# Kernel optimization log

Hardware: AMD Instinct MI355X
Metric: run time of the kernel (lower is better)

The kernel has to match this reference:

```python
import jax, jax.numpy as jnp
import numpy as np

DIM = 2          # num_input_channels
NB = 8           # num_bins (normflows default)
TB = 3.0         # tail_bound
MINW = 1e-3; MINH = 1e-3; MIND = 1e-3
H = 128          # hidden_units
NL = 16          # flow_length
NBLK = 2         # hidden_layers (MADE residual blocks)
PM = 3 * NB - 1  # spline params per dim
DCONST = float(np.log(np.expm1(1.0 - MIND)))  # tail pad constant for derivatives
SQH = float(np.sqrt(H))
LU_EPS = 1e-3

# MADE masks for features=2: input degrees [1,2], all hidden degrees = 1
_M0 = np.zeros((H, DIM), np.float32); _M0[:, 0] = 1.0
_MF = np.zeros((DIM * PM, H), np.float32); _MF[PM:, :] = 1.0
M0 = jnp.asarray(_M0); MF = jnp.asarray(_MF)


def _mlp(x, w1, b1, w2, b2):
    return jax.nn.silu(x @ w1.T + b1) @ w2.T + b2


def _made(zin, W0, b0, Wres, bres, Wf, bf):
    h = zin @ (W0 * M0).T + b0
    for blk in range(NBLK):  # residual blocks (hidden masks all-ones for dim=2)
        t = jax.nn.relu(h)
        t = t @ Wres[blk, 0].T + bres[blk, 0]
        t = jax.nn.relu(t)
        t = t @ Wres[blk, 1].T + bres[blk, 1]
        h = h + t
    return (h @ (Wf * MF).T + bf).reshape(zin.shape[0], DIM, PM)


def _rqs_inverse(y, uw, uh, ud):
    # unconstrained rational-quadratic spline with linear tails, inverse direction
    widths = MINW + (1 - MINW * NB) * jax.nn.softmax(uw, -1)
    cw = jnp.concatenate([jnp.zeros_like(widths[..., :1]), jnp.cumsum(widths, -1)], -1)
    cw = (2 * TB * cw - TB).at[..., 0].set(-TB).at[..., -1].set(TB)
    widths = cw[..., 1:] - cw[..., :-1]
    heights = MINH + (1 - MINH * NB) * jax.nn.softmax(uh, -1)
    ch = jnp.concatenate([jnp.zeros_like(heights[..., :1]), jnp.cumsum(heights, -1)], -1)
    ch = (2 * TB * ch - TB).at[..., 0].set(-TB).at[..., -1].set(TB)
    heights = ch[..., 1:] - ch[..., :-1]
    pad = jnp.full(ud.shape[:-1] + (1,), DCONST, ud.dtype)
    d = MIND + jax.nn.softplus(jnp.concatenate([pad, ud, pad], -1))
    inside = (y >= -TB) & (y <= TB)
    yc = jnp.clip(y, -TB, TB)
    idx = jnp.clip(jnp.sum(yc[..., None] >= ch, -1) - 1, 0, NB - 1)[..., None]
    take = lambda a, i: jnp.take_along_axis(a, i, -1)[..., 0]
    yk = take(ch, idx); hk = take(heights, idx)
    xk = take(cw, idx); wk = take(widths, idx)
    dk = take(d, idx); dk1 = take(d, idx + 1)
    sk = hk / wk; dy = yc - yk; t2 = dk + dk1 - 2 * sk
    a = dy * t2 + hk * (sk - dk)
    b = hk * dk - dy * t2
    c = -sk * dy
    disc = jnp.maximum(b * b - 4 * a * c, 0.0)
    theta = 2 * c / (-b - jnp.sqrt(disc))
    xo = theta * wk + xk
    om = 1 - theta
    denom = sk + t2 * theta * om
    dnum = (sk * sk) * (dk1 * theta * theta + 2 * sk * theta * om + dk * om * om)
    ld_fwd = jnp.log(dnum) - 2 * jnp.log(denom)
    return jnp.where(inside, xo, y), jnp.where(inside, -ld_fwd, 0.0)


def _flow_forward(z_0, x, sigma, n1_w1, n1_b1, n1_w2, n1_b2, n2_w1, n2_b1, n2_w2, n2_b2,
                  made_W0, made_b0, made_Wres, made_bres, made_Wf, made_bf,
                  lu_lower, lu_upper, lu_diag, lu_bias, perms):
    tcond = _mlp(sigma, n1_w1, n1_b1, n1_w2, n1_b2)
    z = _mlp(jnp.concatenate([z_0, x], -1), n2_w1, n2_b1, n2_w2, n2_b2) + tcond
    ld_tot = jnp.zeros(z.shape[0], z.dtype)
    for i in range(NL):
        # AR RQ-spline flow: flow.forward() == sequential inverse of MADE spline
        y = z
        out = jnp.zeros_like(y)
        ldp = jnp.zeros_like(y)
        for _ in range(DIM):
            p = _made(out, made_W0[i], made_b0[i], made_Wres[i], made_bres[i], made_Wf[i], made_bf[i])
            out, ldp = _rqs_inverse(y, p[..., :NB] / SQH, p[..., NB:2 * NB] / SQH, p[..., 2 * NB:])
        ld_tot = ld_tot + ldp.sum(-1)
        # LULinearPermute.forward == LU-linear inverse then permutation inverse
        diag = jax.nn.softplus(lu_diag[i]) + LU_EPS
        Lm = jnp.eye(DIM, dtype=z.dtype).at[1, 0].set(lu_lower[i])
        Um = jnp.diag(diag).at[0, 1].set(lu_upper[i])
        Wm = Lm @ Um
        z = (out - lu_bias[i]) @ jnp.linalg.inv(Wm).T
        ld_tot = ld_tot - jnp.sum(jnp.log(diag))
        z = z[:, perms[i]]
    return z, ld_tot


def setup_inputs() -> dict:
    key = jax.random.key(0)
    ks = jax.random.split(key, 20)
    B = 262144
    f = jnp.float32
    rn = lambda k, s, sc=1.0: jax.random.normal(k, s, dtype=f) * sc
    inp = {}
    inp["z_0"] = rn(ks[0], (B, DIM))
    inp["x"] = rn(ks[1], (B, DIM))
    inp["sigma"] = jax.random.uniform(ks[2], (B, 1), dtype=f)
    inp["n1_w1"] = rn(ks[3], (32, 1), 0.5); inp["n1_b1"] = jnp.zeros((32,), f)
    inp["n1_w2"] = rn(ks[4], (DIM, 32), 0.2); inp["n1_b2"] = jnp.zeros((DIM,), f)
    inp["n2_w1"] = rn(ks[5], (32, 2 * DIM), 0.5); inp["n2_b1"] = jnp.zeros((32,), f)
    inp["n2_w2"] = rn(ks[6], (DIM, 32), 0.2); inp["n2_b2"] = jnp.zeros((DIM,), f)
    inp["made_W0"] = rn(ks[7], (NL, H, DIM), 0.3)
    inp["made_b0"] = rn(ks[8], (NL, H), 0.1)
    inp["made_Wres"] = rn(ks[9], (NL, NBLK, 2, H, H), 0.05)
    inp["made_bres"] = rn(ks[10], (NL, NBLK, 2, H), 0.05)
    inp["made_Wf"] = rn(ks[11], (NL, DIM * PM, H), 0.05)
    inp["made_bf"] = rn(ks[12], (NL, DIM * PM), 0.05)
    inp["lu_lower"] = rn(ks[13], (NL,), 0.3)
    inp["lu_upper"] = rn(ks[14], (NL,), 0.3)
    inp["lu_diag"] = rn(ks[15], (NL, DIM), 0.3) + 0.5413  # softplus^-1(1)
    inp["lu_bias"] = rn(ks[16], (NL, DIM), 0.1)
    inp["perms"] = jnp.asarray(np.stack([[1, 0] if i % 2 else [0, 1] for i in range(NL)]).astype(np.int32))
    return inp


def reference(z_0, x, sigma, n1_w1, n1_b1, n1_w2, n1_b2, n2_w1, n2_b1, n2_w2, n2_b2,
              made_W0, made_b0, made_Wres, made_bres, made_Wf, made_bf,
              lu_lower, lu_upper, lu_diag, lu_bias, perms):
    return _flow_forward(z_0, x, sigma, n1_w1, n1_b1, n1_w2, n1_b2, n2_w1, n2_b1, n2_w2, n2_b2,
                         made_W0, made_b0, made_Wres, made_bres, made_Wf, made_bf,
                         lu_lower, lu_upper, lu_diag, lu_bias, perms)
```

## Files before the change

### kernel.cpp

```cpp
#include <hip/hip_runtime.h>
#include <math.h>

#define NBATCH 262144
#define INVSQH 0.08838834764831845f

#define NPT   2048
#define NGRID 1920
#define TROW  24

#define WT_OFF   0
#define WFT_OFF  4194304
#define WS0_OFF  4456448
#define XS_OFF   4464640
#define BP_OFF   4472832
#define TAB_OFF  4603904
#define REC_OFF  7749632
#define LDC_OFF  7752192

__device__ __forceinline__ float fastrcp(float x) {
#if __has_builtin(__builtin_amdgcn_rcpf)
    return __builtin_amdgcn_rcpf(x);
#else
    return 1.f / x;
#endif
}
__device__ __forceinline__ float fastdiv(float a, float b) { return a * fastrcp(b); }
__device__ __forceinline__ float fastsqrt(float x) {
#if __has_builtin(__builtin_amdgcn_sqrtf)
    return __builtin_amdgcn_sqrtf(x);
#else
    return sqrtf(x);
#endif
}

__device__ __forceinline__ float softplusf(float x) {
    return (x > 15.f) ? x : __logf(1.f + __expf(x));
}

__device__ __forceinline__ float gridval(int i) {
    float v = -56.8f + i * 0.25f;
    if (i >= 192)  v = -8.8f + (i - 192) * 0.0125f;
    if (i >= 1600) v = 9.05f + (i - 1600) * 0.25f;
    if (i >= 1792) v = 58.5f + (i - 1792) * 0.01f;
    return v;
}
__device__ __forceinline__ int cnt_grid_le_exact(float x) {
    int c = 0;
#pragma unroll
    for (int stp = 1024; stp; stp >>= 1) {
        int n = c + stp;
        if (n <= NGRID && gridval(n - 1) <= x) c = n;
    }
    return c;
}
__device__ __forceinline__ int cnt_grid_le_fast(float x) {
    if (x < -56.8f) return 0;
    if (x < -8.8f)  return min((int)floorf((x + 56.8f) * 4.0f) + 1, 192);
    if (x < 9.05f)  return 192 + min((int)floorf((x + 8.8f) * 80.0f) + 1, 1408);
    if (x < 58.5f)  return 1600 + min((int)floorf((x - 9.05f) * 4.0f) + 1, 192);
    return 1792 + min((int)floorf((x - 58.5f) * 100.0f) + 1, 128);
}

__device__ __forceinline__ void rqs_solve(float y, float yc, float yk, float hk, float xk,
                                          float wk, float dk, float dk1,
                                          float& xout, float& ldout)
{
    float sk = fastdiv(hk, wk);
    float dy = yc - yk;
    float t2 = dk + dk1 - 2.f * sk;
    float av = dy * t2 + hk * (sk - dk);
    float bv = hk * dk - dy * t2;
    float cv = -sk * dy;
    float disc = fmaxf(bv * bv - 4.f * av * cv, 0.f);
    float theta = 2.f * cv * fastrcp(-bv - fastsqrt(disc));
    float xo = fmaf(theta, wk, xk);
    float om = 1.f - theta;
    float denom = fmaf(t2, theta * om, sk);
    float dnum = sk * sk * (dk1 * theta * theta + 2.f * sk * theta * om + dk * om * om);
    float rden = fastrcp(denom);
    float ldf = __logf(dnum * rden * rden);
    bool inside = (y >= -3.f) && (y <= 3.f);
    xout  = inside ? xo : y;
    ldout = inside ? -ldf : 0.f;
}

__device__ __forceinline__ void knots_from_p(const float* __restrict__ p,
                                             float* __restrict__ cw,
                                             float* __restrict__ ch,
                                             float* __restrict__ d)
{
    float uw[8], uh[8];
#pragma unroll
    for (int j = 0; j < 8; ++j) uw[j] = p[j] * INVSQH;
#pragma unroll
    for (int j = 0; j < 8; ++j) uh[j] = p[8 + j] * INVSQH;
    float mw = uw[0], mh = uh[0];
#pragma unroll
    for (int j = 1; j < 8; ++j) { mw = fmaxf(mw, uw[j]); mh = fmaxf(mh, uh[j]); }
    float ew[8], eh[8], sw = 0.f, sh = 0.f;
#pragma unroll
    for (int j = 0; j < 8; ++j) {
        ew[j] = __expf(uw[j] - mw); sw += ew[j];
        eh[j] = __expf(uh[j] - mh); sh += eh[j];
    }
    float isw = 0.992f * fastrcp(sw), ish = 0.992f * fastrcp(sh);
    cw[0] = -3.f; ch[0] = -3.f;
    float aw = 0.f, ah = 0.f;
#pragma unroll
    for (int j = 0; j < 8; ++j) {
        aw += 0.001f + ew[j] * isw;
        ah += 0.001f + eh[j] * ish;
        cw[j + 1] = 6.f * aw - 3.f;
        ch[j + 1] = 6.f * ah - 3.f;
    }
    cw[8] = 3.f; ch[8] = 3.f;
    d[0] = 1.f; d[8] = 1.f;
#pragma unroll
    for (int j = 0; j < 7; ++j) d[j + 1] = 0.001f + softplusf(p[16 + j]);
}

__device__ __forceinline__ void rqs_from_knots(float y, const float* __restrict__ cw,
                                               const float* __restrict__ ch,
                                               const float* __restrict__ d,
                                               float& xout, float& ldout)
{
    float yc = fminf(fmaxf(y, -3.f), 3.f);
    float yk = ch[0], hk = ch[1] - ch[0], xk = cw[0], wk = cw[1] - cw[0];
    float dk = d[0], dk1 = d[1];
#pragma unroll
    for (int j = 1; j < 8; ++j) {
        bool cge = (yc >= ch[j]);
        yk  = cge ? ch[j] : yk;
        hk  = cge ? (ch[j + 1] - ch[j]) : hk;
        xk  = cge ? cw[j] : xk;
        wk  = cge ? (cw[j + 1] - cw[j]) : wk;
        dk  = cge ? d[j] : dk;
        dk1 = cge ? d[j + 1] : dk1;
    }
    rqs_solve(y, yc, yk, hk, xk, wk, dk, dk1, xout, ldout);
}

__device__ __forceinline__ void rqs_knots(float y, const float* __restrict__ rec,
                                          float& xout, float& ldout)
{
    rqs_from_knots(y, rec, rec + 9, rec + 18, xout, ldout);
}

extern "C" __global__ __launch_bounds__(256)
void nsf_prep(const float* __restrict__ Wresg, const float* __restrict__ Wfg,
              const float* __restrict__ W0g,  const float* __restrict__ b0g,
              const float* __restrict__ bfg,
              const float* __restrict__ lulg, const float* __restrict__ luug,
              const float* __restrict__ ludg, const float* __restrict__ lubg,
              const int* __restrict__ permsg, char* __restrict__ ws)
{
    const int t = blockIdx.x * 256 + threadIdx.x;
    const int stride = gridDim.x * 256;
    float* WT  = (float*)(ws + WT_OFF);
    float* WFT = (float*)(ws + WFT_OFF);
    float* ws0 = (float*)(ws + WS0_OFF);
    float* xsg = (float*)(ws + XS_OFF);
    float* bp  = (float*)(ws + BP_OFF);

    for (int e = t; e < 16 * 4 * 16384; e += stride) {
        int sidx = e >> 14, rem = e & 16383, k = rem >> 7, u = rem & 127;
        WT[e] = Wresg[sidx * 16384 + u * 128 + k];
    }
    for (int e = t; e < 16 * 128 * 32; e += stride) {
        int L = e >> 12, rem = e & 4095, k = rem >> 5, o = rem & 31;
        WFT[e] = (o < 23) ? Wfg[(L * 46 + 23 + o) * 128 + k] : 0.f;
    }
    for (int e = t; e < 2048; e += stride) ws0[e] = W0g[2 * e];

    if (blockIdx.x < 16) {
        __shared__ float xr[128], xsL[128];
        const int L = blockIdx.x, tid = threadIdx.x;
        if (tid < 128) {
            float aa = W0g[L * 256 + 2 * tid];
            float cc = b0g[L * 128 + tid];
            float xv = -cc / aa;
            xr[tid] = (fabsf(xv) < 56.0f) ? xv : (57.0f + tid * 0.01f);
        }
        __syncthreads();
        if (tid < 128) {
            float v = xr[tid];
            int rank = 0;
            for (int j = 0; j < 128; ++j) {
                float u = xr[j];
                rank += (u < v || (u == v && j < tid)) ? 1 : 0;
            }
            xsL[rank] = v;
        }
        __syncthreads();
        if (tid < 128) {
            float v = xsL[tid];
            xsg[L * 128 + tid] = v;
            bp[L * NPT + tid + cnt_grid_le_exact(v)] = v;
        }
        for (int i = tid; i < NGRID; i += 256) {
            float g = gridval(i);
            int cl = 0;
#pragma unroll
            for (int stp = 64; stp; stp >>= 1)
                if (xsL[cl + stp - 1] < g) cl += stp;
            bp[L * NPT + i + cl] = g;
        }
        if (tid == 0) {
            float* rec = (float*)(ws + REC_OFF) + L * 40;
            const float* p = bfg + L * 46;
            for (int half = 0; half < 2; ++half) {
                float u[8], m = -1e30f;
                for (int j = 0; j < 8; ++j) { u[j] = p[half * 8 + j] * INVSQH; m = fmaxf(m, u[j]); }
                float e[8], ssum = 0.f;
                for (int j = 0; j < 8; ++j) { e[j] = expf(u[j] - m); ssum += e[j]; }
                float cum = 0.f;
                rec[half * 9 + 0] = -3.f;
                for (int j = 0; j < 8; ++j) {
                    cum += 0.001f + 0.992f * e[j] / ssum;
                    rec[half * 9 + 1 + j] = 6.f * cum - 3.f;
                }
                rec[half * 9 + 8] = 3.f;
            }
            rec[18] = 1.f; rec[26] = 1.f;
            for (int j = 0; j < 7; ++j) {
                float x = p[16 + j];
                rec[19 + j] = 0.001f + ((x > 15.f) ? x : log1pf(expf(x)));
            }
            float x0 = ludg[2 * L], x1 = ludg[2 * L + 1];
            float dg0 = 0.001f + ((x0 > 15.f) ? x0 : log1pf(expf(x0)));
            float dg1 = 0.001f + ((x1 > 15.f) ? x1 : log1pf(expf(x1)));
            float ll = lulg[L], uu = luug[L];
            float det = dg0 * dg1;
            float c00 = (ll * uu + dg1) / det, c01 = -uu / det;
            float c10 = -ll / dg1, c11 = 1.f / dg1;
            int pa = permsg[2 * L], pb = permsg[2 * L + 1];
            rec[27] = pa ? c10 : c00; rec[28] = pa ? c11 : c01;
            rec[29] = pb ? c10 : c00; rec[30] = pb ? c11 : c01;
            rec[31] = lubg[2 * L];    rec[32] = lubg[2 * L + 1];
        }
        if (L == 0 && tid == 32) {
            float ssum = 0.f;
            for (int l2 = 0; l2 < 16; ++l2) {
                float x0 = ludg[2 * l2], x1 = ludg[2 * l2 + 1];
                float dg0 = 0.001f + ((x0 > 15.f) ? x0 : log1pf(expf(x0)));
                float dg1 = 0.001f + ((x1 > 15.f) ? x1 : log1pf(expf(x1)));
                ssum += logf(dg0) + logf(dg1);
            }
            *(float*)(ws + LDC_OFF) = ssum;
        }
    }
}

extern "C" __global__ __launch_bounds__(256, 2)
void nsf_eval(const float* __restrict__ bresg, const float* __restrict__ b0g,
              const float* __restrict__ bfg, char* __restrict__ ws)
{
    __shared__ float R[128 * 68];
    __shared__ float p1sh[64 * 24];
    const int tid = threadIdx.x;
    const int lane = tid & 63, w = tid >> 6;
    const int u0 = w * 32 + (lane & 3) * 8;
    const int p0 = (lane >> 2) * 4;
    const int L = blockIdx.x >> 5;
    const int pb = (blockIdx.x & 31) << 6;

    const float* WT  = (const float*)(ws + WT_OFF);
    const float* WFT = (const float*)(ws + WFT_OFF);
    const float* ws0 = (const float*)(ws + WS0_OFF);
    const float* bp  = (const float*)(ws + BP_OFF);
    float* tab = (float*)(ws + TAB_OFF);

    float H[8][4];
    {
        float4 s4 = *(const float4*)(bp + L * NPT + pb + p0);
        float sp[4] = {s4.x, s4.y, s4.z, s4.w};
        float4 a0 = *(const float4*)(ws0 + L * 128 + u0);
        float4 a1 = *(const float4*)(ws0 + L * 128 + u0 + 4);
        float4 c0 = *(const float4*)(b0g + L * 128 + u0);
        float4 c1 = *(const float4*)(b0g + L * 128 + u0 + 4);
        float aj[8] = {a0.x, a0.y, a0.z, a0.w, a1.x, a1.y, a1.z, a1.w};
        float cj[8] = {c0.x, c0.y, c0.z, c0.w, c1.x, c1.y, c1.z, c1.w};
#pragma unroll
        for (int j = 0; j < 8; ++j) {
#pragma unroll
            for (int p = 0; p < 4; ++p) H[j][p] = fmaf(aj[j], sp[p], cj[j]);
            float4 v = {fmaxf(H[j][0], 0.f), fmaxf(H[j][1], 0.f),
                        fmaxf(H[j][2], 0.f), fmaxf(H[j][3], 0.f)};
            *(float4*)(&R[(u0 + j) * 68 + p0]) = v;
        }
    }
    __syncthreads();

#pragma unroll 1
    for (int st = 0; st < 4; ++st) {
        const float* Wst = WT + (L * 4 + st) * 16384;
        const float* bb  = bresg + (L * 4 + st) * 128;
        float acc[8][4];
        {
            float4 b0v = *(const float4*)(bb + u0);
            float4 b1v = *(const float4*)(bb + u0 + 4);
            float bj[8] = {b0v.x, b0v.y, b0v.z, b0v.w, b1v.x, b1v.y, b1v.z, b1v.w};
#pragma unroll
            for (int j = 0; j < 8; ++j)
#pragma unroll
                for (int p = 0; p < 4; ++p) acc[j][p] = bj[j];
        }
#pragma unroll 4
        for (int k = 0; k < 128; ++k) {
            float4 w0 = *(const float4*)(Wst + k * 128 + u0);
            float4 w1 = *(const float4*)(Wst + k * 128 + u0 + 4);
            float4 r  = *(const float4*)(&R[k * 68 + p0]);
            float wj[8] = {w0.x, w0.y, w0.z, w0.w, w1.x, w1.y, w1.z, w1.w};
            float rp[4] = {r.x, r.y, r.z, r.w};
#pragma unroll
            for (int j = 0; j < 8; ++j)
#pragma unroll
                for (int p = 0; p < 4; ++p)
                    acc[j][p] = fmaf(wj[j], rp[p], acc[j][p]);
        }
        if (st == 1 || st == 3) {
#pragma unroll
            for (int j = 0; j < 8; ++j)
#pragma unroll
                for (int p = 0; p < 4; ++p) H[j][p] += acc[j][p];
        }
        __syncthreads();
#pragma unroll
        for (int j = 0; j < 8; ++j) {
            float4 v;
            if (st == 0 || st == 2) {
                v = (float4){fmaxf(acc[j][0], 0.f), fmaxf(acc[j][1], 0.f),
                             fmaxf(acc[j][2], 0.f), fmaxf(acc[j][3], 0.f)};
            } else if (st == 1) {
                v = (float4){fmaxf(H[j][0], 0.f), fmaxf(H[j][1], 0.f),
                             fmaxf(H[j][2], 0.f), fmaxf(H[j][3], 0.f)};
            } else {
                v = (float4){H[j][0], H[j][1], H[j][2], H[j][3]};
            }
            *(float4*)(&R[(u0 + j) * 68 + p0]) = v;
        }
        __syncthreads();
    }

    {
        const int o = tid & 31, pg8 = tid >> 5;
        float pacc[8];
#pragma unroll
        for (int p = 0; p < 8; ++p) pacc[p] = 0.f;
#pragma unroll 4
        for (int k = 0; k < 128; ++k) {
            float wf = WFT[(L * 128 + k) * 32 + o];
            float4 ra = *(const float4*)(&R[k * 68 + pg8 * 8]);
            float4 rb = *(const float4*)(&R[k * 68 + pg8 * 8 + 4]);
            pacc[0] = fmaf(wf, ra.x, pacc[0]);
            pacc[1] = fmaf(wf, ra.y, pacc[1]);
            pacc[2] = fmaf(wf, ra.z, pacc[2]);
            pacc[3] = fmaf(wf, ra.w, pacc[3]);
            pacc[4] = fmaf(wf, rb.x, pacc[4]);
            pacc[5] = fmaf(wf, rb.y, pacc[5]);
            pacc[6] = fmaf(wf, rb.z, pacc[6]);
            pacc[7] = fmaf(wf, rb.w, pacc[7]);
        }
        if (o < 23) {
            float bias = bfg[L * 46 + 23 + o];
#pragma unroll
            for (int p = 0; p < 8; ++p)
                p1sh[(pg8 * 8 + p) * 24 + o] = pacc[p] + bias;
        }
    }
    __syncthreads();

    if (tid < 64) {
        float pp[23];
#pragma unroll
        for (int j = 0; j < 23; ++j) pp[j] = p1sh[tid * 24 + j];
        float cw[9], ch[9], d[9];
        knots_from_p(pp, cw, ch, d);
        float out[24];
#pragma unroll
        for (int i = 0; i < 8; ++i) out[i] = cw[i + 1];
#pragma unroll
        for (int i = 0; i < 8; ++i) out[8 + i] = ch[i + 1];
#pragma unroll
        for (int i = 0; i < 7; ++i) out[16 + i] = d[i + 1];
        out[23] = bp[L * NPT + pb + tid];
        float4* dst = (float4*)(tab + (L * NPT + pb + tid) * TROW);
#pragma unroll
        for (int i = 0; i < 6; ++i)
            dst[i] = ((const float4*)out)[i];
    }
}

extern "C" __global__ __launch_bounds__(256)
void nsf_main(const float* __restrict__ z0g, const float* __restrict__ xg,
              const float* __restrict__ sgg,
              const float* __restrict__ n1w1, const float* __restrict__ n1b1,
              const float* __restrict__ n1w2, const float* __restrict__ n1b2,
              const float* __restrict__ n2w1, const float* __restrict__ n2b1,
              const float* __restrict__ n2w2, const float* __restrict__ n2b2,
              const char* __restrict__ ws, float* __restrict__ outg)
{
    __shared__ float xsl[16 * 128];
    __shared__ float recs_s[16 * 40];

    const float* xsg  = (const float*)(ws + XS_OFF);
    const float* tab  = (const float*)(ws + TAB_OFF);
    const float* recg = (const float*)(ws + REC_OFF);

    const int tid = threadIdx.x;
    const int s = blockIdx.x * 256 + tid;

    for (int i = tid; i < 2048; i += 256) xsl[i] = xsg[i];
    for (int i = tid; i < 640; i += 256) recs_s[i] = recg[i];
    __syncthreads();

    float zz0, zz1, ld = 0.f;
    {
        float za = z0g[2 * s], zb = z0g[2 * s + 1];
        float xa = xg[2 * s],  xb = xg[2 * s + 1];
        float sg = sgg[s];
        float t0 = n1b2[0], t1 = n1b2[1];
#pragma unroll
        for (int m = 0; m < 32; ++m) {
            float hm = fmaf(sg, n1w1[m], n1b1[m]);
            hm = hm * fastrcp(1.f + __expf(-hm));
            t0 = fmaf(hm, n1w2[m], t0);
            t1 = fmaf(hm, n1w2[32 + m], t1);
        }
        float u0 = n2b2[0], u1 = n2b2[1];
#pragma unroll
        for (int m = 0; m < 32; ++m) {
            float hm = za * n2w1[4 * m] + zb * n2w1[4 * m + 1]
                     + xa * n2w1[4 * m + 2] + xb * n2w1[4 * m + 3] + n2b1[m];
            hm = hm * fastrcp(1.f + __expf(-hm));
            u0 = fmaf(hm, n2w2[m], u0);
            u1 = fmaf(hm, n2w2[32 + m], u1);
        }
        zz0 = u0 + t0; zz1 = u1 + t1;
    }

    for (int L = 0; L < 16; ++L) {
        const float* rec = recs_s + L * 40;
        float out0, ldp0;
        rqs_knots(zz0, rec, out0, ldp0);

        int cg = cnt_grid_le_fast(out0);
        const float* xs = xsl + L * 128;
        int cx = 0;
#pragma unroll
        for (int stp = 64; stp; stp >>= 1)
            if (xs[cx + stp - 1] <= out0) cx += stp;
        int pos = cg + cx - 1;
        pos = max(0, min(pos, NPT - 2));

        const float4* r4 = (const float4*)(tab + (L * NPT + pos) * TROW);
        float f0[24], f1[24];
#pragma unroll
        for (int i = 0; i < 6; ++i) {
            float4 a = r4[i], b = r4[i + 6];
            f0[4 * i] = a.x; f0[4 * i + 1] = a.y; f0[4 * i + 2] = a.z; f0[4 * i + 3] = a.w;
            f1[4 * i] = b.x; f1[4 * i + 1] = b.y; f1[4 * i + 2] = b.z; f1[4 * i + 3] = b.w;
        }
        float e0 = f0[23], e1 = f1[23];
        float de = e1 - e0;
        float tt = (de > 1e-9f) ? (out0 - e0) * fastrcp(de) : 0.f;

        float cw[9], ch[9], d[9];
        cw[0] = -3.f; ch[0] = -3.f; d[0] = 1.f; d[8] = 1.f;
#pragma unroll
        for (int i = 0; i < 8; ++i) cw[i + 1] = fmaf(tt, f1[i] - f0[i], f0[i]);
#pragma unroll
        for (int i = 0; i < 8; ++i) ch[i + 1] = fmaf(tt, f1[8 + i] - f0[8 + i], f0[8 + i]);
#pragma unroll
        for (int i = 0; i < 7; ++i) d[i + 1] = fmaf(tt, f1[16 + i] - f0[16 + i], f0[16 + i]);

        float out1, ldp1;
        rqs_from_knots(zz1, cw, ch, d, out1, ldp1);
        ld += ldp0 + ldp1;

        float v0 = out0 - rec[31], v1 = out1 - rec[32];
        zz0 = fmaf(v0, rec[27], v1 * rec[28]);
        zz1 = fmaf(v0, rec[29], v1 * rec[30]);
    }

    float ldc = *(const float*)(ws + LDC_OFF);
    outg[2 * s] = zz0;
    outg[2 * s + 1] = zz1;
    outg[2 * NBATCH + s] = ld - ldc;
}

extern "C" void kernel_launch(void* const* d_in, const int* in_sizes, int n_in,
                              void* d_out, int out_size, void* d_ws, size_t ws_size,
                              hipStream_t stream)
{
    const float* z0g  = (const float*)d_in[0];
    const float* xg   = (const float*)d_in[1];
    const float* sgg  = (const float*)d_in[2];
    const float* n1w1 = (const float*)d_in[3];
    const float* n1b1 = (const float*)d_in[4];
    const float* n1w2 = (const float*)d_in[5];
    const float* n1b2 = (const float*)d_in[6];
    const float* n2w1 = (const float*)d_in[7];
    const float* n2b1 = (const float*)d_in[8];
    const float* n2w2 = (const float*)d_in[9];
    const float* n2b2 = (const float*)d_in[10];
    const float* W0g  = (const float*)d_in[11];
    const float* b0g  = (const float*)d_in[12];
    const float* Wres = (const float*)d_in[13];
    const float* bres = (const float*)d_in[14];
    const float* Wfg  = (const float*)d_in[15];
    const float* bfg  = (const float*)d_in[16];
    const float* lul  = (const float*)d_in[17];
    const float* luu  = (const float*)d_in[18];
    const float* lud  = (const float*)d_in[19];
    const float* lub  = (const float*)d_in[20];
    const int*   perms= (const int*)d_in[21];
    float* outg = (float*)d_out;
    char* ws = (char*)d_ws;

    nsf_prep<<<256, 256, 0, stream>>>(Wres, Wfg, W0g, b0g, bfg, lul, luu, lud, lub, perms, ws);
    nsf_eval<<<512, 256, 0, stream>>>(bres, b0g, bfg, ws);
    nsf_main<<<NBATCH / 256, 256, 0, stream>>>(z0g, xg, sgg,
                                               n1w1, n1b1, n1w2, n1b2,
                                               n2w1, n2b1, n2w2, n2b2,
                                               ws, outg);
}
```

Baseline: 289.9 us.

## Drop ReLU-kink breakpoints from table grid and tile prep/eval for more parallelism

```diff
diff --git a/kernel.cpp b/kernel.cpp
--- a/kernel.cpp
+++ b/kernel.cpp
@@ -11,11 +11,9 @@
 #define WT_OFF   0
 #define WFT_OFF  4194304
 #define WS0_OFF  4456448
-#define XS_OFF   4464640
-#define BP_OFF   4472832
-#define TAB_OFF  4603904
-#define REC_OFF  7749632
-#define LDC_OFF  7752192
+#define TAB_OFF  4464640
+#define REC_OFF  7610368
+#define LDC_OFF  7612928
 
 __device__ __forceinline__ float fastrcp(float x) {
 #if __has_builtin(__builtin_amdgcn_rcpf)
@@ -43,15 +41,6 @@
     if (i >= 1600) v = 9.05f + (i - 1600) * 0.25f;
     if (i >= 1792) v = 58.5f + (i - 1792) * 0.01f;
     return v;
-}
-__device__ __forceinline__ int cnt_grid_le_exact(float x) {
-    int c = 0;
-#pragma unroll
-    for (int stp = 1024; stp; stp >>= 1) {
-        int n = c + stp;
-        if (n <= NGRID && gridval(n - 1) <= x) c = n;
-    }
-    return c;
 }
 __device__ __forceinline__ int cnt_grid_le_fast(float x) {
     if (x < -56.8f) return 0;
@@ -154,126 +143,110 @@
               const float* __restrict__ ludg, const float* __restrict__ lubg,
               const int* __restrict__ permsg, char* __restrict__ ws)
 {
-    const int t = blockIdx.x * 256 + threadIdx.x;
-    const int stride = gridDim.x * 256;
+    const int b = blockIdx.x, tid = threadIdx.x;
     float* WT  = (float*)(ws + WT_OFF);
     float* WFT = (float*)(ws + WFT_OFF);
     float* ws0 = (float*)(ws + WS0_OFF);
-    float* xsg = (float*)(ws + XS_OFF);
-    float* bp  = (float*)(ws + BP_OFF);
-
-    for (int e = t; e < 16 * 4 * 16384; e += stride) {
-        int sidx = e >> 14, rem = e & 16383, k = rem >> 7, u = rem & 127;
-        WT[e] = Wresg[sidx * 16384 + u * 128 + k];
-    }
-    for (int e = t; e < 16 * 128 * 32; e += stride) {
-        int L = e >> 12, rem = e & 4095, k = rem >> 5, o = rem & 31;
-        WFT[e] = (o < 23) ? Wfg[(L * 46 + 23 + o) * 128 + k] : 0.f;
-    }
-    for (int e = t; e < 2048; e += stride) ws0[e] = W0g[2 * e];
-
-    if (blockIdx.x < 16) {
-        __shared__ float xr[128], xsL[128];
-        const int L = blockIdx.x, tid = threadIdx.x;
-        if (tid < 128) {
-            float aa = W0g[L * 256 + 2 * tid];
-            float cc = b0g[L * 128 + tid];
-            float xv = -cc / aa;
-            xr[tid] = (fabsf(xv) < 56.0f) ? xv : (57.0f + tid * 0.01f);
+
+    if (b < 256) {
+        __shared__ float T[64][65];
+        const int mat = b >> 2, tr = (b >> 1) & 1, tc = b & 1;
+        const float* src = Wresg + mat * 16384;
+        float* dst = WT + mat * 16384;
+        const int r = tid >> 2, q = tid & 3;
+#pragma unroll
+        for (int i = 0; i < 4; ++i) {
+            int c4 = q * 4 + i;
+            float4 v = *(const float4*)(src + (tr * 64 + r) * 128 + tc * 64 + c4 * 4);
+            T[r][c4 * 4 + 0] = v.x; T[r][c4 * 4 + 1] = v.y;
+            T[r][c4 * 4 + 2] = v.z; T[r][c4 * 4 + 3] = v.w;
         }
         __syncthreads();
-        if (tid < 128) {
-            float v = xr[tid];
-            int rank = 0;
-            for (int j = 0; j < 128; ++j) {
-                float u = xr[j];
-                rank += (u < v || (u == v && j < tid)) ? 1 : 0;
+        const int kk = tid >> 2;
+#pragma unroll
+        for (int i = 0; i < 4; ++i) {
+            int u4 = q * 4 + i;
+            float4 v;
+            v.x = T[u4 * 4 + 0][kk]; v.y = T[u4 * 4 + 1][kk];
+            v.z = T[u4 * 4 + 2][kk]; v.w = T[u4 * 4 + 3][kk];
+            *(float4*)(dst + (tc * 64 + kk) * 128 + tr * 64 + u4 * 4) = v;
+        }
+        return;
+    }
+
+    const int L = b - 256;
+    for (int e = tid; e < 4096; e += 256) {
+        int k = e >> 5, o = e & 31;
+        WFT[L * 4096 + e] = (o < 23) ? Wfg[(L * 46 + 23 + o) * 128 + k] : 0.f;
+    }
+    if (tid < 128) ws0[L * 128 + tid] = W0g[L * 256 + 2 * tid];
+
+    if (tid == 0) {
+        float* rec = (float*)(ws + REC_OFF) + L * 40;
+        const float* p = bfg + L * 46;
+        for (int half = 0; half < 2; ++half) {
+            float u[8], m = -1e30f;
+            for (int j = 0; j < 8; ++j) { u[j] = p[half * 8 + j] * INVSQH; m = fmaxf(m, u[j]); }
+            float e[8], ssum = 0.f;
+            for (int j = 0; j < 8; ++j) { e[j] = expf(u[j] - m); ssum += e[j]; }
+            float cum = 0.f;
+            rec[half * 9 + 0] = -3.f;
+            for (int j = 0; j < 8; ++j) {
+                cum += 0.001f + 0.992f * e[j] / ssum;
+                rec[half * 9 + 1 + j] = 6.f * cum - 3.f;
             }
-            xsL[rank] = v;
-        }
-        __syncthreads();
-        if (tid < 128) {
-            float v = xsL[tid];
-            xsg[L * 128 + tid] = v;
-            bp[L * NPT + tid + cnt_grid_le_exact(v)] = v;
-        }
-        for (int i = tid; i < NGRID; i += 256) {
-            float g = gridval(i);
-            int cl = 0;
-#pragma unroll
-            for (int stp = 64; stp; stp >>= 1)
-                if (xsL[cl + stp - 1] < g) cl += stp;
-            bp[L * NPT + i + cl] = g;
-        }
-        if (tid == 0) {
-            float* rec = (float*)(ws + REC_OFF) + L * 40;
-            const float* p = bfg + L * 46;
-            for (int half = 0; half < 2; ++half) {
-                float u[8], m = -1e30f;
-                for (int j = 0; j < 8; ++j) { u[j] = p[half * 8 + j] * INVSQH; m = fmaxf(m, u[j]); }
-                float e[8], ssum = 0.f;
-                for (int j = 0; j < 8; ++j) { e[j] = expf(u[j] - m); ssum += e[j]; }
-                float cum = 0.f;
-                rec[half * 9 + 0] = -3.f;
-                for (int j = 0; j < 8; ++j) {
-                    cum += 0.001f + 0.992f * e[j] / ssum;
-                    rec[half * 9 + 1 + j] = 6.f * cum - 3.f;
-                }
-                rec[half * 9 + 8] = 3.f;
-            }
-            rec[18] = 1.f; rec[26] = 1.f;
-            for (int j = 0; j < 7; ++j) {
-                float x = p[16 + j];
-                rec[19 + j] = 0.001f + ((x > 15.f) ? x : log1pf(expf(x)));
-            }
-            float x0 = ludg[2 * L], x1 = ludg[2 * L + 1];
+            rec[half * 9 + 8] = 3.f;
+        }
+        rec[18] = 1.f; rec[26] = 1.f;
+        for (int j = 0; j < 7; ++j) {
+            float x = p[16 + j];
+            rec[19 + j] = 0.001f + ((x > 15.f) ? x : log1pf(expf(x)));
+        }
+        float x0 = ludg[2 * L], x1 = ludg[2 * L + 1];
+        float dg0 = 0.001f + ((x0 > 15.f) ? x0 : log1pf(expf(x0)));
+        float dg1 = 0.001f + ((x1 > 15.f) ? x1 : log1pf(expf(x1)));
+        float ll = lulg[L], uu = luug[L];
+        float det = dg0 * dg1;
+        float c00 = (ll * uu + dg1) / det, c01 = -uu / det;
+        float c10 = -ll / dg1, c11 = 1.f / dg1;
+        int pa = permsg[2 * L], pb2 = permsg[2 * L + 1];
+        rec[27] = pa ? c10 : c00;  rec[28] = pa ? c11 : c01;
+        rec[29] = pb2 ? c10 : c00; rec[30] = pb2 ? c11 : c01;
+        rec[31] = lubg[2 * L];     rec[32] = lubg[2 * L + 1];
+    }
+    if (L == 0 && tid == 32) {
+        float ssum = 0.f;
+        for (int l2 = 0; l2 < 16; ++l2) {
+            float x0 = ludg[2 * l2], x1 = ludg[2 * l2 + 1];
             float dg0 = 0.001f + ((x0 > 15.f) ? x0 : log1pf(expf(x0)));
             float dg1 = 0.001f + ((x1 > 15.f) ? x1 : log1pf(expf(x1)));
-            float ll = lulg[L], uu = luug[L];
-            float det = dg0 * dg1;
-            float c00 = (ll * uu + dg1) / det, c01 = -uu / det;
-            float c10 = -ll / dg1, c11 = 1.f / dg1;
-            int pa = permsg[2 * L], pb = permsg[2 * L + 1];
-            rec[27] = pa ? c10 : c00; rec[28] = pa ? c11 : c01;
-            rec[29] = pb ? c10 : c00; rec[30] = pb ? c11 : c01;
-            rec[31] = lubg[2 * L];    rec[32] = lubg[2 * L + 1];
-        }
-        if (L == 0 && tid == 32) {
-            float ssum = 0.f;
-            for (int l2 = 0; l2 < 16; ++l2) {
-                float x0 = ludg[2 * l2], x1 = ludg[2 * l2 + 1];
-                float dg0 = 0.001f + ((x0 > 15.f) ? x0 : log1pf(expf(x0)));
-                float dg1 = 0.001f + ((x1 > 15.f) ? x1 : log1pf(expf(x1)));
-                ssum += logf(dg0) + logf(dg1);
-            }
-            *(float*)(ws + LDC_OFF) = ssum;
-        }
-    }
-}
-
-extern "C" __global__ __launch_bounds__(256, 2)
+            ssum += logf(dg0) + logf(dg1);
+        }
+        *(float*)(ws + LDC_OFF) = ssum;
+    }
+}
+
+extern "C" __global__ __launch_bounds__(256, 4)
 void nsf_eval(const float* __restrict__ bresg, const float* __restrict__ b0g,
               const float* __restrict__ bfg, char* __restrict__ ws)
 {
-    __shared__ float R[128 * 68];
-    __shared__ float p1sh[64 * 24];
+    __shared__ float R[128 * 36];
+    __shared__ float p1sh[32 * 24];
     const int tid = threadIdx.x;
     const int lane = tid & 63, w = tid >> 6;
     const int u0 = w * 32 + (lane & 3) * 8;
-    const int p0 = (lane >> 2) * 4;
-    const int L = blockIdx.x >> 5;
-    const int pb = (blockIdx.x & 31) << 6;
+    const int p0 = (lane >> 2) * 2;
+    const int L = blockIdx.x >> 6;
+    const int pb = (blockIdx.x & 63) << 5;
 
     const float* WT  = (const float*)(ws + WT_OFF);
     const float* WFT = (const float*)(ws + WFT_OFF);
     const float* ws0 = (const float*)(ws + WS0_OFF);
-    const float* bp  = (const float*)(ws + BP_OFF);
     float* tab = (float*)(ws + TAB_OFF);
 
-    float H[8][4];
+    float H[8][2];
     {
-        float4 s4 = *(const float4*)(bp + L * NPT + pb + p0);
-        float sp[4] = {s4.x, s4.y, s4.z, s4.w};
+        float sp[2] = {gridval(pb + p0), gridval(pb + p0 + 1)};
         float4 a0 = *(const float4*)(ws0 + L * 128 + u0);
         float4 a1 = *(const float4*)(ws0 + L * 128 + u0 + 4);
         float4 c0 = *(const float4*)(b0g + L * 128 + u0);
@@ -283,10 +256,9 @@
 #pragma unroll
         for (int j = 0; j < 8; ++j) {
 #pragma unroll
-            for (int p = 0; p < 4; ++p) H[j][p] = fmaf(aj[j], sp[p], cj[j]);
-            float4 v = {fmaxf(H[j][0], 0.f), fmaxf(H[j][1], 0.f),
-                        fmaxf(H[j][2], 0.f), fmaxf(H[j][3], 0.f)};
-            *(float4*)(&R[(u0 + j) * 68 + p0]) = v;
+            for (int p = 0; p < 2; ++p) H[j][p] = fmaf(aj[j], sp[p], cj[j]);
+            float2 v = {fmaxf(H[j][0], 0.f), fmaxf(H[j][1], 0.f)};
+            *(float2*)(&R[(u0 + j) * 36 + p0]) = v;
         }
     }
     __syncthreads();
@@ -295,82 +267,64 @@
     for (int st = 0; st < 4; ++st) {
         const float* Wst = WT + (L * 4 + st) * 16384;
         const float* bb  = bresg + (L * 4 + st) * 128;
-        float acc[8][4];
+        float acc[8][2];
         {
             float4 b0v = *(const float4*)(bb + u0);
             float4 b1v = *(const float4*)(bb + u0 + 4);
             float bj[8] = {b0v.x, b0v.y, b0v.z, b0v.w, b1v.x, b1v.y, b1v.z, b1v.w};
 #pragma unroll
-            for (int j = 0; j < 8; ++j)
-#pragma unroll
-                for (int p = 0; p < 4; ++p) acc[j][p] = bj[j];
+            for (int j = 0; j < 8; ++j) { acc[j][0] = bj[j]; acc[j][1] = bj[j]; }
         }
 #pragma unroll 4
         for (int k = 0; k < 128; ++k) {
             float4 w0 = *(const float4*)(Wst + k * 128 + u0);
             float4 w1 = *(const float4*)(Wst + k * 128 + u0 + 4);
-            float4 r  = *(const float4*)(&R[k * 68 + p0]);
+            float2 r  = *(const float2*)(&R[k * 36 + p0]);
             float wj[8] = {w0.x, w0.y, w0.z, w0.w, w1.x, w1.y, w1.z, w1.w};
-            float rp[4] = {r.x, r.y, r.z, r.w};
-#pragma unroll
-            for (int j = 0; j < 8; ++j)
-#pragma unroll
-                for (int p = 0; p < 4; ++p)
-                    acc[j][p] = fmaf(wj[j], rp[p], acc[j][p]);
+#pragma unroll
+            for (int j = 0; j < 8; ++j) {
+                acc[j][0] = fmaf(wj[j], r.x, acc[j][0]);
+                acc[j][1] = fmaf(wj[j], r.y, acc[j][1]);
+            }
         }
         if (st == 1 || st == 3) {
 #pragma unroll
-            for (int j = 0; j < 8; ++j)
-#pragma unroll
-                for (int p = 0; p < 4; ++p) H[j][p] += acc[j][p];
+            for (int j = 0; j < 8; ++j) { H[j][0] += acc[j][0]; H[j][1] += acc[j][1]; }
         }
         __syncthreads();
 #pragma unroll
         for (int j = 0; j < 8; ++j) {
-            float4 v;
-            if (st == 0 || st == 2) {
-                v = (float4){fmaxf(acc[j][0], 0.f), fmaxf(acc[j][1], 0.f),
-                             fmaxf(acc[j][2], 0.f), fmaxf(acc[j][3], 0.f)};
-            } else if (st == 1) {
-                v = (float4){fmaxf(H[j][0], 0.f), fmaxf(H[j][1], 0.f),
-                             fmaxf(H[j][2], 0.f), fmaxf(H[j][3], 0.f)};
-            } else {
-                v = (float4){H[j][0], H[j][1], H[j][2], H[j][3]};
-            }
-            *(float4*)(&R[(u0 + j) * 68 + p0]) = v;
+            float2 v;
+            if (st == 0 || st == 2)      v = {fmaxf(acc[j][0], 0.f), fmaxf(acc[j][1], 0.f)};
+            else if (st == 1)            v = {fmaxf(H[j][0], 0.f),  fmaxf(H[j][1], 0.f)};
+            else                         v = {H[j][0], H[j][1]};
+            *(float2*)(&R[(u0 + j) * 36 + p0]) = v;
         }
         __syncthreads();
     }
 
     {
-        const int o = tid & 31, pg8 = tid >> 5;
-        float pacc[8];
-#pragma unroll
-        for (int p = 0; p < 8; ++p) pacc[p] = 0.f;
+        const int o = tid & 31, pg4 = tid >> 5;
+        float pacc[4] = {0.f, 0.f, 0.f, 0.f};
 #pragma unroll 4
         for (int k = 0; k < 128; ++k) {
             float wf = WFT[(L * 128 + k) * 32 + o];
-            float4 ra = *(const float4*)(&R[k * 68 + pg8 * 8]);
-            float4 rb = *(const float4*)(&R[k * 68 + pg8 * 8 + 4]);
+            float4 ra = *(const float4*)(&R[k * 36 + pg4 * 4]);
             pacc[0] = fmaf(wf, ra.x, pacc[0]);
             pacc[1] = fmaf(wf, ra.y, pacc[1]);
             pacc[2] = fmaf(wf, ra.z, pacc[2]);
             pacc[3] = fmaf(wf, ra.w, pacc[3]);
-            pacc[4] = fmaf(wf, rb.x, pacc[4]);
-            pacc[5] = fmaf(wf, rb.y, pacc[5]);
-            pacc[6] = fmaf(wf, rb.z, pacc[6]);
-            pacc[7] = fmaf(wf, rb.w, pacc[7]);
         }
         if (o < 23) {
             float bias = bfg[L * 46 + 23 + o];
 #pragma unroll
-            for (int p = 0; p < 8; ++p)
-                p1sh[(pg8 * 8 + p) * 24 + o] = pacc[p] + bias;
+            for (int p = 0; p < 4; ++p)
+                p1sh[(pg4 * 4 + p) * 24 + o] = pacc[p] + bias;
         }
     }
     __syncthreads();
 
-    if (tid < 64) {
+    if (tid < 32) {
         float pp[23];
 #pragma unroll
         for (int j = 0; j < 23; ++j) pp[j] = p1sh[tid * 24 + j];
@@ -383,7 +337,7 @@
         for (int i = 0; i < 8; ++i) out[8 + i] = ch[i + 1];
 #pragma unroll
         for (int i = 0; i < 7; ++i) out[16 + i] = d[i + 1];
-        out[23] = bp[L * NPT + pb + tid];
+        out[23] = gridval(pb + tid);
         float4* dst = (float4*)(tab + (L * NPT + pb + tid) * TROW);
 #pragma unroll
         for (int i = 0; i < 6; ++i)
@@ -391,7 +345,7 @@
     }
 }
 
-extern "C" __global__ __launch_bounds__(256)
+extern "C" __global__ __launch_bounds__(256, 4)
 void nsf_main(const float* __restrict__ z0g, const float* __restrict__ xg,
               const float* __restrict__ sgg,
               const float* __restrict__ n1w1, const float* __restrict__ n1b1,
@@ -400,17 +354,14 @@
               const float* __restrict__ n2w2, const float* __restrict__ n2b2,
               const char* __restrict__ ws, float* __restrict__ outg)
 {
-    __shared__ float xsl[16 * 128];
     __shared__ float recs_s[16 * 40];
 
-    const float* xsg  = (const float*)(ws + XS_OFF);
     const float* tab  = (const float*)(ws + TAB_OFF);
     const float* recg = (const float*)(ws + REC_OFF);
 
     const int tid = threadIdx.x;
     const int s = blockIdx.x * 256 + tid;
 
-    for (int i = tid; i < 2048; i += 256) xsl[i] = xsg[i];
     for (int i = tid; i < 640; i += 256) recs_s[i] = recg[i];
     __syncthreads();
 
@@ -444,35 +395,37 @@
         float out0, ldp0;
         rqs_knots(zz0, rec, out0, ldp0);
 
-        int cg = cnt_grid_le_fast(out0);
-        const float* xs = xsl + L * 128;
-        int cx = 0;
-#pragma unroll
-        for (int stp = 64; stp; stp >>= 1)
-            if (xs[cx + stp - 1] <= out0) cx += stp;
-        int pos = cg + cx - 1;
-        pos = max(0, min(pos, NPT - 2));
+        int pos = min(max(cnt_grid_le_fast(out0) - 1, 0), NGRID - 2);
 
         const float4* r4 = (const float4*)(tab + (L * NPT + pos) * TROW);
-        float f0[24], f1[24];
-#pragma unroll
-        for (int i = 0; i < 6; ++i) {
-            float4 a = r4[i], b = r4[i + 6];
-            f0[4 * i] = a.x; f0[4 * i + 1] = a.y; f0[4 * i + 2] = a.z; f0[4 * i + 3] = a.w;
-            f1[4 * i] = b.x; f1[4 * i + 1] = b.y; f1[4 * i + 2] = b.z; f1[4 * i + 3] = b.w;
-        }
-        float e0 = f0[23], e1 = f1[23];
+        float4 q0[6], q1[6];
+#pragma unroll
+        for (int i = 0; i < 6; ++i) { q0[i] = r4[i]; q1[i] = r4[i + 6]; }
+
+        float e0 = q0[5].w, e1 = q1[5].w;
         float de = e1 - e0;
         float tt = (de > 1e-9f) ? (out0 - e0) * fastrcp(de) : 0.f;
 
         float cw[9], ch[9], d[9];
         cw[0] = -3.f; ch[0] = -3.f; d[0] = 1.f; d[8] = 1.f;
 #pragma unroll
-        for (int i = 0; i < 8; ++i) cw[i + 1] = fmaf(tt, f1[i] - f0[i], f0[i]);
-#pragma unroll
-        for (int i = 0; i < 8; ++i) ch[i + 1] = fmaf(tt, f1[8 + i] - f0[8 + i], f0[8 + i]);
-#pragma unroll
-        for (int i = 0; i < 7; ++i) d[i + 1] = fmaf(tt, f1[16 + i] - f0[16 + i], f0[16 + i]);
+        for (int i = 0; i < 2; ++i) {
+            cw[4 * i + 1] = fmaf(tt, q1[i].x - q0[i].x, q0[i].x);
+            cw[4 * i + 2] = fmaf(tt, q1[i].y - q0[i].y, q0[i].y);
+            cw[4 * i + 3] = fmaf(tt, q1[i].z - q0[i].z, q0[i].z);
+            cw[4 * i + 4] = fmaf(tt, q1[i].w - q0[i].w, q0[i].w);
+            ch[4 * i + 1] = fmaf(tt, q1[i + 2].x - q0[i + 2].x, q0[i + 2].x);
+            ch[4 * i + 2] = fmaf(tt, q1[i + 2].y - q0[i + 2].y, q0[i + 2].y);
+            ch[4 * i + 3] = fmaf(tt, q1[i + 2].z - q0[i + 2].z, q0[i + 2].z);
+            ch[4 * i + 4] = fmaf(tt, q1[i + 2].w - q0[i + 2].w, q0[i + 2].w);
+        }
+        d[1] = fmaf(tt, q1[4].x - q0[4].x, q0[4].x);
+        d[2] = fmaf(tt, q1[4].y - q0[4].y, q0[4].y);
+        d[3] = fmaf(tt, q1[4].z - q0[4].z, q0[4].z);
+        d[4] = fmaf(tt, q1[4].w - q0[4].w, q0[4].w);
+        d[5] = fmaf(tt, q1[5].x - q0[5].x, q0[5].x);
+        d[6] = fmaf(tt, q1[5].y - q0[5].y, q0[5].y);
+        d[7] = fmaf(tt, q1[5].z - q0[5].z, q0[5].z);
 
         float out1, ldp1;
         rqs_from_knots(zz1, cw, ch, d, out1, ldp1);
@@ -518,8 +471,8 @@
     float* outg = (float*)d_out;
     char* ws = (char*)d_ws;
 
-    nsf_prep<<<256, 256, 0, stream>>>(Wres, Wfg, W0g, b0g, bfg, lul, luu, lud, lub, perms, ws);
-    nsf_eval<<<512, 256, 0, stream>>>(bres, b0g, bfg, ws);
+    nsf_prep<<<272, 256, 0, stream>>>(Wres, Wfg, W0g, b0g, bfg, lul, luu, lud, lub, perms, ws);
+    nsf_eval<<<1024, 256, 0, stream>>>(bres, b0g, bfg, ws);
     nsf_main<<<NBATCH / 256, 256, 0, stream>>>(z0g, xg, sgg,
                                                n1w1, n1b1, n1w2, n1b2,
                                                n2w1, n2b1, n2w2, n2b2,
```

Result: slower. 331.4 us (+14.3%).
